# Kernel optimization log

Hardware: AMD Instinct MI355X
Metric: run time of the kernel (lower is better)

The kernel has to match this reference:

```python
import jax, jax.numpy as jnp
import numpy as np

B, D_IN, D_H, W_RANK, U_RANK = 8192, 1024, 2048, 256, 256


def setup_inputs() -> dict:
    key = jax.random.key(0)
    ks = jax.random.split(key, 6)
    return {
        "input": jax.random.normal(ks[0], (B, D_IN), dtype=jnp.float32),
        "state": jax.random.normal(ks[1], (B, D_H), dtype=jnp.float32),
        "W1": 0.1 * jax.random.normal(ks[2], (W_RANK, D_IN), dtype=jnp.float32),
        "W2": 0.1 * jax.random.normal(ks[3], (D_H, W_RANK), dtype=jnp.float32),
        "U1": 0.1 * jax.random.normal(ks[4], (U_RANK, D_H), dtype=jnp.float32),
        "U2": 0.1 * jax.random.normal(ks[5], (D_H, U_RANK), dtype=jnp.float32),
        "bias_gate": jnp.ones((1, D_H), dtype=jnp.float32),
        "bias_update": jnp.ones((1, D_H), dtype=jnp.float32),
        "zeta": 1.0 * jnp.ones((1, 1), dtype=jnp.float32),
        "nu": -4.0 * jnp.ones((1, 1), dtype=jnp.float32),
    }


def reference(input, state, W1, W2, U1, U2, bias_gate, bias_update, zeta, nu):
    # Low-rank projections: Wx = x @ W1^T @ W2^T ; Uh = h @ U1^T @ U2^T
    wx = jnp.einsum("bi,ri->br", input, W1)          # [B, wRank]
    wx = jnp.einsum("br,hr->bh", wx, W2)             # [B, H]
    uh = jnp.einsum("bh,rh->br", state, U1)          # [B, uRank]
    uh = jnp.einsum("br,hr->bh", uh, U2)             # [B, H]
    pre = wx + uh                                     # shared pre-activation
    z = jax.nn.sigmoid(pre + bias_gate)               # gate (sigmoid)
    h_cand = jnp.tanh(pre + bias_update)              # update (tanh)
    # h_t = z*h_{t-1} + (sigmoid(zeta)*(1-z) + sigmoid(nu)) * h_cand
    new_h = z * state + (jax.nn.sigmoid(zeta) * (1.0 - z) + jax.nn.sigmoid(nu)) * h_cand
    return new_h
```

## Files before the change

### kernel.cpp

```cpp
#include <hip/hip_runtime.h>
#include <hip/hip_fp16.h>
#include <cstdint>
#include <cstddef>


typedef _Float16 half8 __attribute__((ext_vector_type(8)));
typedef float f32x4 __attribute__((ext_vector_type(4)));

#define DIN 1024
#define DH 2048
#define RK 256
#define RB_LD 768
#define OFF_W1H 0
#define OFF_U1H 262144
#define OFF_W2H 786432
#define OFF_U2H 1310720

__device__ __forceinline__ half8 cvt8(const float4 a, const float4 b) {
  half8 h;
  h[0] = (_Float16)a.x; h[1] = (_Float16)a.y; h[2] = (_Float16)a.z; h[3] = (_Float16)a.w;
  h[4] = (_Float16)b.x; h[5] = (_Float16)b.y; h[6] = (_Float16)b.z; h[7] = (_Float16)b.w;
  return h;
}

__global__ __launch_bounds__(256)
void fgrnn_prep(const float* __restrict__ W1, const float* __restrict__ U1,
                const float* __restrict__ W2, const float* __restrict__ U2,
                _Float16* __restrict__ wb) {
  const int q = blockIdx.x * 256 + threadIdx.x;
  const float* src;
  int rel;
  if (q < 65536) { src = W1; rel = q; }
  else if (q < 196608) { src = U1; rel = q - 65536; }
  else if (q < 327680) { src = W2; rel = q - 196608; }
  else { src = U2; rel = q - 327680; }
  const float4 v = reinterpret_cast<const float4*>(src)[rel];
  union { _Float16 h[4]; uint2 u; } cv;
  cv.h[0] = (_Float16)v.x; cv.h[1] = (_Float16)v.y;
  cv.h[2] = (_Float16)v.z; cv.h[3] = (_Float16)v.w;
  reinterpret_cast<uint2*>(wb)[q] = cv.u;
}

__global__ __launch_bounds__(512)
void fgrnn_stage1(const float* __restrict__ x, const float* __restrict__ h,
                  const _Float16* __restrict__ wb, _Float16* __restrict__ rbuf) {
  const int bid = blockIdx.x;
  const int grp = bid >> 7;
  const int mtile = bid & 127;
  const float* A = grp ? h : x;
  const _Float16* Bw = grp ? (wb + OFF_U1H) : (wb + OFF_W1H);
  const int KA = grp ? DH : DIN;
  const int kbase = (grp == 2) ? 1024 : 0;
  const int colbase = grp << 8;
  const int row0 = mtile * 64;

  __shared__ _Float16 As[64 * 64];
  __shared__ _Float16 Bs[256 * 64];

  const int tid = threadIdx.x;
  const int lane = tid & 63;
  const int w = tid >> 6;
  const int wr = w >> 2, wc = w & 3;

  f32x4 acc[2][4];
#pragma unroll
  for (int i = 0; i < 2; ++i)
#pragma unroll
    for (int j = 0; j < 4; ++j) acc[i][j] = (f32x4){0.f, 0.f, 0.f, 0.f};

  const int sr = tid >> 3;
  const int sc = (tid & 7) * 8;

  float4 pa0, pa1;
  half8 pb[4];

  auto LOADG = [&](int it) {
    const int k0 = kbase + it * 64;
    const float* sa = A + (size_t)(row0 + sr) * KA + k0 + sc;
    pa0 = *reinterpret_cast<const float4*>(sa);
    pa1 = *reinterpret_cast<const float4*>(sa + 4);
#pragma unroll
    for (int j = 0; j < 4; ++j)
      pb[j] = *reinterpret_cast<const half8*>(Bw + (size_t)(j * 64 + sr) * KA + k0 + sc);
  };
  auto STORE = [&]() {
    *reinterpret_cast<half8*>(&As[sr * 64 + (sc ^ ((sr & 7) << 3))]) = cvt8(pa0, pa1);
#pragma unroll
    for (int j = 0; j < 4; ++j) {
      const int r = j * 64 + sr;
      *reinterpret_cast<half8*>(&Bs[r * 64 + (sc ^ ((r & 7) << 3))]) = pb[j];
    }
  };

  LOADG(0);
  STORE();
  __syncthreads();

  for (int it = 0; it < 16; ++it) {
    const bool more = (it + 1 < 16);
    if (more) LOADG(it + 1);
#pragma unroll
    for (int kk = 0; kk < 64; kk += 32) {
      half8 af[2], bf[4];
#pragma unroll
      for (int mi = 0; mi < 2; ++mi) {
        const int r = wr * 32 + mi * 16 + (lane & 15);
        af[mi] = *reinterpret_cast<const half8*>(
            &As[r * 64 + ((kk + 8 * (lane >> 4)) ^ ((r & 7) << 3))]);
      }
#pragma unroll
      for (int ni = 0; ni < 4; ++ni) {
        const int r = wc * 64 + ni * 16 + (lane & 15);
        bf[ni] = *reinterpret_cast<const half8*>(
            &Bs[r * 64 + ((kk + 8 * (lane >> 4)) ^ ((r & 7) << 3))]);
      }
#pragma unroll
      for (int mi = 0; mi < 2; ++mi)
#pragma unroll
        for (int ni = 0; ni < 4; ++ni)
          acc[mi][ni] =
              __builtin_amdgcn_mfma_f32_16x16x32_f16(af[mi], bf[ni], acc[mi][ni], 0, 0, 0);
    }
    if (more) {
      __syncthreads();
      STORE();
    }
    __syncthreads();
  }

#pragma unroll
  for (int mi = 0; mi < 2; ++mi)
#pragma unroll
    for (int ni = 0; ni < 4; ++ni)
#pragma unroll
      for (int e = 0; e < 4; ++e) {
        const int row = row0 + wr * 32 + mi * 16 + 4 * (lane >> 4) + e;
        const int col = colbase + wc * 64 + ni * 16 + (lane & 15);
        rbuf[(size_t)row * RB_LD + col] = (_Float16)acc[mi][ni][e];
      }
}

__global__ __launch_bounds__(256)
void fgrnn_stage2(const _Float16* __restrict__ rbuf, const _Float16* __restrict__ wb,
                  const float* __restrict__ state,
                  const float* __restrict__ bg, const float* __restrict__ bu,
                  const float* __restrict__ zeta, const float* __restrict__ nu,
                  float* __restrict__ out) {
  const int bid = blockIdx.x;
  const int mtile = bid >> 4;
  const int ntile = bid & 15;
  const int row0 = mtile * 64;
  const int col0 = ntile * 128;
  const _Float16* W2h = wb + OFF_W2H;
  const _Float16* U2h = wb + OFF_U2H;

  __shared__ _Float16 As[64 * 64];
  __shared__ _Float16 Bs[128 * 64];

  const int tid = threadIdx.x;
  const int lane = tid & 63;
  const int w = tid >> 6;
  const int wr = w >> 1, wc = w & 1;

  f32x4 acc[2][4];
#pragma unroll
  for (int i = 0; i < 2; ++i)
#pragma unroll
    for (int j = 0; j < 4; ++j) acc[i][j] = (f32x4){0.f, 0.f, 0.f, 0.f};

  const int sr = tid >> 3;
  const int sc = (tid & 7) * 8;

  half8 pa[2], pa2[2], pb[4];

  auto LOADG = [&](int it) {
    const int k0 = it * 64;
#pragma unroll
    for (int j = 0; j < 2; ++j) {
      const _Float16* p = rbuf + (size_t)(row0 + j * 32 + sr) * RB_LD + k0 + sc;
      pa[j] = *reinterpret_cast<const half8*>(p);
      if (k0 >= 256) pa2[j] = *reinterpret_cast<const half8*>(p + 256);
    }
    const _Float16* Bh = (k0 < 256) ? W2h : U2h;
    const int kb = k0 & 255;
#pragma unroll
    for (int j = 0; j < 4; ++j)
      pb[j] = *reinterpret_cast<const half8*>(Bh + (size_t)(col0 + j * 32 + sr) * RK + kb + sc);
  };
  auto STORE = [&](int it) {
    const int k0 = it * 64;
#pragma unroll
    for (int j = 0; j < 2; ++j) {
      const int r = j * 32 + sr;
      half8 v = pa[j];
      if (k0 >= 256) v = v + pa2[j];
      *reinterpret_cast<half8*>(&As[r * 64 + (sc ^ ((r & 7) << 3))]) = v;
    }
#pragma unroll
    for (int j = 0; j < 4; ++j) {
      const int r = j * 32 + sr;
      *reinterpret_cast<half8*>(&Bs[r * 64 + (sc ^ ((r & 7) << 3))]) = pb[j];
    }
  };

  LOADG(0);
  STORE(0);
  __syncthreads();

  for (int it = 0; it < 8; ++it) {
    const bool more = (it + 1 < 8);
    if (more) LOADG(it + 1);
#pragma unroll
    for (int kk = 0; kk < 64; kk += 32) {
      half8 af[2], bf[4];
#pragma unroll
      for (int mi = 0; mi < 2; ++mi) {
        const int r = wr * 32 + mi * 16 + (lane & 15);
        af[mi] = *reinterpret_cast<const half8*>(
            &As[r * 64 + ((kk + 8 * (lane >> 4)) ^ ((r & 7) << 3))]);
      }
#pragma unroll
      for (int ni = 0; ni < 4; ++ni) {
        const int r = wc * 64 + ni * 16 + (lane & 15);
        bf[ni] = *reinterpret_cast<const half8*>(
            &Bs[r * 64 + ((kk + 8 * (lane >> 4)) ^ ((r & 7) << 3))]);
      }
#pragma unroll
      for (int mi = 0; mi < 2; ++mi)
#pragma unroll
        for (int ni = 0; ni < 4; ++ni)
          acc[mi][ni] =
              __builtin_amdgcn_mfma_f32_16x16x32_f16(af[mi], bf[ni], acc[mi][ni], 0, 0, 0);
    }
    if (more) {
      __syncthreads();
      STORE(it + 1);
    }
    __syncthreads();
  }

  const float LOG2E = 1.44269504f;
  const float sz = __builtin_amdgcn_rcpf(1.f + __builtin_amdgcn_exp2f(-zeta[0] * LOG2E));
  const float sn = __builtin_amdgcn_rcpf(1.f + __builtin_amdgcn_exp2f(-nu[0] * LOG2E));
#pragma unroll
  for (int mi = 0; mi < 2; ++mi)
#pragma unroll
    for (int ni = 0; ni < 4; ++ni) {
      const int col = col0 + wc * 64 + ni * 16 + (lane & 15);
      const float bgc = bg[col];
      const float buc = bu[col];
#pragma unroll
      for (int e = 0; e < 4; ++e) {
        const int row = row0 + wr * 32 + mi * 16 + 4 * (lane >> 4) + e;
        const float pre = acc[mi][ni][e];
        const float zg =
            __builtin_amdgcn_rcpf(1.f + __builtin_amdgcn_exp2f(-(pre + bgc) * LOG2E));
        const float hc =
            1.f - 2.f * __builtin_amdgcn_rcpf(
                            1.f + __builtin_amdgcn_exp2f((pre + buc) * (2.f * LOG2E)));
        const float sv = state[(size_t)row * DH + col];
        out[(size_t)row * DH + col] = zg * sv + (sz * (1.f - zg) + sn) * hc;
      }
    }
}

extern "C" void kernel_launch(void* const* d_in, const int* in_sizes, int n_in,
                              void* d_out, int out_size, void* d_ws, size_t ws_size,
                              hipStream_t stream) {
  const float* input = (const float*)d_in[0];
  const float* state = (const float*)d_in[1];
  const float* W1 = (const float*)d_in[2];
  const float* W2 = (const float*)d_in[3];
  const float* U1 = (const float*)d_in[4];
  const float* U2 = (const float*)d_in[5];
  const float* bg = (const float*)d_in[6];
  const float* bu = (const float*)d_in[7];
  const float* zeta = (const float*)d_in[8];
  const float* nu = (const float*)d_in[9];
  float* out = (float*)d_out;
  _Float16* rbuf = (_Float16*)d_ws;
  _Float16* wb = (_Float16*)d_ws + (size_t)8192 * 768;

  fgrnn_prep<<<1792, 256, 0, stream>>>(W1, U1, W2, U2, wb);
  fgrnn_stage1<<<384, 512, 0, stream>>>(input, state, wb, rbuf);
  fgrnn_stage2<<<2048, 256, 0, stream>>>(rbuf, wb, state, bg, bu, zeta, nu, out);
}
```

Baseline: 77.87 us.

## Split stage1 K dimension into more partial groups with larger M tiles and XCD-aware block remap

```diff
diff --git a/kernel.cpp b/kernel.cpp
--- a/kernel.cpp
+++ b/kernel.cpp
@@ -10,11 +10,11 @@
 #define DIN 1024
 #define DH 2048
 #define RK 256
-#define RB_LD 768
 #define OFF_W1H 0
 #define OFF_U1H 262144
 #define OFF_W2H 786432
 #define OFF_U2H 1310720
+#define WB_HALVES 1835008
 
 __device__ __forceinline__ half8 cvt8(const float4 a, const float4 b) {
   half8 h;
@@ -41,20 +41,29 @@
   reinterpret_cast<uint2*>(wb)[q] = cv.u;
 }
 
+template <int G>
 __global__ __launch_bounds__(512)
 void fgrnn_stage1(const float* __restrict__ x, const float* __restrict__ h,
                   const _Float16* __restrict__ wb, _Float16* __restrict__ rbuf) {
+  constexpr int KL = (G == 6) ? 512 : 256;
+  constexpr int ITERS = KL / 64;
+  constexpr int GX = 1024 / KL;
+  constexpr int RBLD = G * 256;
+  constexpr int NB = G * 64;
+
   const int bid = blockIdx.x;
-  const int grp = bid >> 7;
-  const int mtile = bid & 127;
-  const float* A = grp ? h : x;
-  const _Float16* Bw = grp ? (wb + OFF_U1H) : (wb + OFF_W1H);
-  const int KA = grp ? DH : DIN;
-  const int kbase = (grp == 2) ? 1024 : 0;
-  const int colbase = grp << 8;
-  const int row0 = mtile * 64;
-
-  __shared__ _Float16 As[64 * 64];
+  const int L = (bid & 7) * (NB / 8) + (bid >> 3);
+  const int g = L >> 6;
+  const int mtile = L & 63;
+  const bool isx = g < GX;
+  const float* A = isx ? x : h;
+  const int KA = isx ? DIN : DH;
+  const int kbase = (isx ? g : (g - GX)) * KL;
+  const _Float16* Bw = wb + (isx ? OFF_W1H : OFF_U1H);
+  const int row0 = mtile * 128;
+  const int colbase = g * 256;
+
+  __shared__ _Float16 As[128 * 64];
   __shared__ _Float16 Bs[256 * 64];
 
   const int tid = threadIdx.x;
@@ -62,29 +71,37 @@
   const int w = tid >> 6;
   const int wr = w >> 2, wc = w & 3;
 
-  f32x4 acc[2][4];
-#pragma unroll
-  for (int i = 0; i < 2; ++i)
+  f32x4 acc[4][4];
+#pragma unroll
+  for (int i = 0; i < 4; ++i)
 #pragma unroll
     for (int j = 0; j < 4; ++j) acc[i][j] = (f32x4){0.f, 0.f, 0.f, 0.f};
 
   const int sr = tid >> 3;
   const int sc = (tid & 7) * 8;
 
-  float4 pa0, pa1;
+  float4 pa4[2][2];
   half8 pb[4];
 
   auto LOADG = [&](int it) {
     const int k0 = kbase + it * 64;
-    const float* sa = A + (size_t)(row0 + sr) * KA + k0 + sc;
-    pa0 = *reinterpret_cast<const float4*>(sa);
-    pa1 = *reinterpret_cast<const float4*>(sa + 4);
+#pragma unroll
+    for (int j = 0; j < 2; ++j) {
+      const float* s = A + (size_t)(row0 + j * 64 + sr) * KA + k0 + sc;
+      pa4[j][0] = *reinterpret_cast<const float4*>(s);
+      pa4[j][1] = *reinterpret_cast<const float4*>(s + 4);
+    }
 #pragma unroll
     for (int j = 0; j < 4; ++j)
       pb[j] = *reinterpret_cast<const half8*>(Bw + (size_t)(j * 64 + sr) * KA + k0 + sc);
   };
   auto STORE = [&]() {
-    *reinterpret_cast<half8*>(&As[sr * 64 + (sc ^ ((sr & 7) << 3))]) = cvt8(pa0, pa1);
+#pragma unroll
+    for (int j = 0; j < 2; ++j) {
+      const int r = j * 64 + sr;
+      *reinterpret_cast<half8*>(&As[r * 64 + (sc ^ ((r & 7) << 3))]) =
+          cvt8(pa4[j][0], pa4[j][1]);
+    }
 #pragma unroll
     for (int j = 0; j < 4; ++j) {
       const int r = j * 64 + sr;
@@ -96,15 +113,15 @@
   STORE();
   __syncthreads();
 
-  for (int it = 0; it < 16; ++it) {
-    const bool more = (it + 1 < 16);
+  for (int it = 0; it < ITERS; ++it) {
+    const bool more = (it + 1 < ITERS);
     if (more) LOADG(it + 1);
 #pragma unroll
     for (int kk = 0; kk < 64; kk += 32) {
-      half8 af[2], bf[4];
-#pragma unroll
-      for (int mi = 0; mi < 2; ++mi) {
-        const int r = wr * 32 + mi * 16 + (lane & 15);
+      half8 af[4], bf[4];
+#pragma unroll
+      for (int mi = 0; mi < 4; ++mi) {
+        const int r = wr * 64 + mi * 16 + (lane & 15);
         af[mi] = *reinterpret_cast<const half8*>(
             &As[r * 64 + ((kk + 8 * (lane >> 4)) ^ ((r & 7) << 3))]);
       }
@@ -115,7 +132,7 @@
             &Bs[r * 64 + ((kk + 8 * (lane >> 4)) ^ ((r & 7) << 3))]);
       }
 #pragma unroll
-      for (int mi = 0; mi < 2; ++mi)
+      for (int mi = 0; mi < 4; ++mi)
 #pragma unroll
         for (int ni = 0; ni < 4; ++ni)
           acc[mi][ni] =
@@ -129,26 +146,32 @@
   }
 
 #pragma unroll
-  for (int mi = 0; mi < 2; ++mi)
+  for (int mi = 0; mi < 4; ++mi)
 #pragma unroll
     for (int ni = 0; ni < 4; ++ni)
 #pragma unroll
       for (int e = 0; e < 4; ++e) {
-        const int row = row0 + wr * 32 + mi * 16 + 4 * (lane >> 4) + e;
+        const int row = row0 + wr * 64 + mi * 16 + 4 * (lane >> 4) + e;
         const int col = colbase + wc * 64 + ni * 16 + (lane & 15);
-        rbuf[(size_t)row * RB_LD + col] = (_Float16)acc[mi][ni][e];
-      }
-}
-
+        rbuf[(size_t)row * RBLD + col] = (_Float16)acc[mi][ni][e];
+      }
+}
+
+template <int G>
 __global__ __launch_bounds__(256)
 void fgrnn_stage2(const _Float16* __restrict__ rbuf, const _Float16* __restrict__ wb,
                   const float* __restrict__ state,
                   const float* __restrict__ bg, const float* __restrict__ bu,
                   const float* __restrict__ zeta, const float* __restrict__ nu,
                   float* __restrict__ out) {
+  constexpr int GX = (G == 6) ? 2 : 4;
+  constexpr int GH = G - GX;
+  constexpr int RBLD = G * 256;
+
   const int bid = blockIdx.x;
-  const int mtile = bid >> 4;
-  const int ntile = bid & 15;
+  const int L = (bid & 7) * 256 + (bid >> 3);
+  const int mtile = L >> 4;
+  const int ntile = L & 15;
   const int row0 = mtile * 64;
   const int col0 = ntile * 128;
   const _Float16* W2h = wb + OFF_W2H;
@@ -171,17 +194,22 @@
   const int sr = tid >> 3;
   const int sc = (tid & 7) * 8;
 
-  half8 pa[2], pa2[2], pb[4];
+  half8 pa[2][GH];
+  half8 pb[4];
 
   auto LOADG = [&](int it) {
     const int k0 = it * 64;
+    const bool iswx = (k0 < 256);
+    const int cb = iswx ? k0 : (GX * 256 + (k0 - 256));
+    const int np = iswx ? GX : GH;
 #pragma unroll
     for (int j = 0; j < 2; ++j) {
-      const _Float16* p = rbuf + (size_t)(row0 + j * 32 + sr) * RB_LD + k0 + sc;
-      pa[j] = *reinterpret_cast<const half8*>(p);
-      if (k0 >= 256) pa2[j] = *reinterpret_cast<const half8*>(p + 256);
-    }
-    const _Float16* Bh = (k0 < 256) ? W2h : U2h;
+      const _Float16* p = rbuf + (size_t)(row0 + j * 32 + sr) * RBLD + cb + sc;
+#pragma unroll
+      for (int q = 0; q < GH; ++q)
+        if (q < np) pa[j][q] = *reinterpret_cast<const half8*>(p + q * 256);
+    }
+    const _Float16* Bh = iswx ? W2h : U2h;
     const int kb = k0 & 255;
 #pragma unroll
     for (int j = 0; j < 4; ++j)
@@ -189,11 +217,14 @@
   };
   auto STORE = [&](int it) {
     const int k0 = it * 64;
+    const int np = (k0 < 256) ? GX : GH;
 #pragma unroll
     for (int j = 0; j < 2; ++j) {
+      half8 v = pa[j][0];
+#pragma unroll
+      for (int q = 1; q < GH; ++q)
+        if (q < np) v = v + pa[j][q];
       const int r = j * 32 + sr;
-      half8 v = pa[j];
-      if (k0 >= 256) v = v + pa2[j];
       *reinterpret_cast<half8*>(&As[r * 64 + (sc ^ ((r & 7) << 3))]) = v;
     }
 #pragma unroll
@@ -278,10 +309,19 @@
   const float* zeta = (const float*)d_in[8];
   const float* nu = (const float*)d_in[9];
   float* out = (float*)d_out;
+
+  const size_t need12 = ((size_t)8192 * 3072 + WB_HALVES) * 2;
   _Float16* rbuf = (_Float16*)d_ws;
-  _Float16* wb = (_Float16*)d_ws + (size_t)8192 * 768;
-
-  fgrnn_prep<<<1792, 256, 0, stream>>>(W1, U1, W2, U2, wb);
-  fgrnn_stage1<<<384, 512, 0, stream>>>(input, state, wb, rbuf);
-  fgrnn_stage2<<<2048, 256, 0, stream>>>(rbuf, wb, state, bg, bu, zeta, nu, out);
-}
+
+  if (ws_size >= need12) {
+    _Float16* wb = rbuf + (size_t)8192 * 3072;
+    fgrnn_prep<<<1792, 256, 0, stream>>>(W1, U1, W2, U2, wb);
+    fgrnn_stage1<12><<<768, 512, 0, stream>>>(input, state, wb, rbuf);
+    fgrnn_stage2<12><<<2048, 256, 0, stream>>>(rbuf, wb, state, bg, bu, zeta, nu, out);
+  } else {
+    _Float16* wb = rbuf + (size_t)8192 * 1536;
+    fgrnn_prep<<<1792, 256, 0, stream>>>(W1, U1, W2, U2, wb);
+    fgrnn_stage1<6><<<384, 512, 0, stream>>>(input, state, wb, rbuf);
+    fgrnn_stage2<6><<<2048, 256, 0, stream>>>(rbuf, wb, state, bg, bu, zeta, nu, out);
+  }
+}
```

Result: slower. 101.7 us (+30.6%).

## Double-buffer stage1 LDS, enlarge state-GEMM M tiles, swizzle stage2 block order

Applied to the files above, without the earlier changes.

```diff
diff --git a/kernel.cpp b/kernel.cpp
--- a/kernel.cpp
+++ b/kernel.cpp
@@ -10,11 +10,12 @@
 #define DIN 1024
 #define DH 2048
 #define RK 256
-#define RB_LD 768
+#define RBLD 768
 #define OFF_W1H 0
 #define OFF_U1H 262144
 #define OFF_W2H 786432
 #define OFF_U2H 1310720
+#define WB_HALVES 1835008
 
 __device__ __forceinline__ half8 cvt8(const float4 a, const float4 b) {
   half8 h;
@@ -41,103 +42,135 @@
   reinterpret_cast<uint2*>(wb)[q] = cv.u;
 }
 
-__global__ __launch_bounds__(512)
-void fgrnn_stage1(const float* __restrict__ x, const float* __restrict__ h,
-                  const _Float16* __restrict__ wb, _Float16* __restrict__ rbuf) {
-  const int bid = blockIdx.x;
-  const int grp = bid >> 7;
-  const int mtile = bid & 127;
-  const float* A = grp ? h : x;
-  const _Float16* Bw = grp ? (wb + OFF_U1H) : (wb + OFF_W1H);
-  const int KA = grp ? DH : DIN;
-  const int kbase = (grp == 2) ? 1024 : 0;
-  const int colbase = grp << 8;
-  const int row0 = mtile * 64;
-
-  __shared__ _Float16 As[64 * 64];
-  __shared__ _Float16 Bs[256 * 64];
+template <int MI>
+__device__ __forceinline__ void s1_body(
+    const float* __restrict__ A, const int KA, const int kbase,
+    const _Float16* __restrict__ Bw, _Float16* __restrict__ rbuf,
+    const int row0, const int colbase,
+    _Float16* __restrict__ AsBase, _Float16* __restrict__ BsBase) {
+  constexpr int APASS = MI / 2;
+  constexpr int ASTRIDE = MI * 32 * 64;
+  constexpr int BSTRIDE = 256 * 64;
 
   const int tid = threadIdx.x;
   const int lane = tid & 63;
   const int w = tid >> 6;
   const int wr = w >> 2, wc = w & 3;
-
-  f32x4 acc[2][4];
-#pragma unroll
-  for (int i = 0; i < 2; ++i)
-#pragma unroll
-    for (int j = 0; j < 4; ++j) acc[i][j] = (f32x4){0.f, 0.f, 0.f, 0.f};
-
   const int sr = tid >> 3;
   const int sc = (tid & 7) * 8;
 
-  float4 pa0, pa1;
-  half8 pb[4];
-
-  auto LOADG = [&](int it) {
+  f32x4 acc[MI][4];
+#pragma unroll
+  for (int i = 0; i < MI; ++i)
+#pragma unroll
+    for (int j = 0; j < 4; ++j) acc[i][j] = (f32x4){0.f, 0.f, 0.f, 0.f};
+
+  float4 raE[APASS][2], raO[APASS][2];
+  half8 rbE[4], rbO[4];
+
+  auto LOADG = [&](float4 (&ra)[APASS][2], half8 (&rb)[4], int it) {
     const int k0 = kbase + it * 64;
-    const float* sa = A + (size_t)(row0 + sr) * KA + k0 + sc;
-    pa0 = *reinterpret_cast<const float4*>(sa);
-    pa1 = *reinterpret_cast<const float4*>(sa + 4);
+#pragma unroll
+    for (int j = 0; j < APASS; ++j) {
+      const float* s = A + (size_t)(row0 + j * 64 + sr) * KA + k0 + sc;
+      ra[j][0] = *reinterpret_cast<const float4*>(s);
+      ra[j][1] = *reinterpret_cast<const float4*>(s + 4);
+    }
 #pragma unroll
     for (int j = 0; j < 4; ++j)
-      pb[j] = *reinterpret_cast<const half8*>(Bw + (size_t)(j * 64 + sr) * KA + k0 + sc);
-  };
-  auto STORE = [&]() {
-    *reinterpret_cast<half8*>(&As[sr * 64 + (sc ^ ((sr & 7) << 3))]) = cvt8(pa0, pa1);
+      rb[j] = *reinterpret_cast<const half8*>(Bw + (size_t)(j * 64 + sr) * KA + k0 + sc);
+  };
+  auto STORE = [&](const float4 (&ra)[APASS][2], const half8 (&rb)[4],
+                   _Float16* as, _Float16* bs) {
+#pragma unroll
+    for (int j = 0; j < APASS; ++j) {
+      const int r = j * 64 + sr;
+      *reinterpret_cast<half8*>(&as[r * 64 + (sc ^ ((r & 7) << 3))]) =
+          cvt8(ra[j][0], ra[j][1]);
+    }
 #pragma unroll
     for (int j = 0; j < 4; ++j) {
       const int r = j * 64 + sr;
-      *reinterpret_cast<half8*>(&Bs[r * 64 + (sc ^ ((r & 7) << 3))]) = pb[j];
-    }
-  };
-
-  LOADG(0);
-  STORE();
-  __syncthreads();
-
-  for (int it = 0; it < 16; ++it) {
-    const bool more = (it + 1 < 16);
-    if (more) LOADG(it + 1);
+      *reinterpret_cast<half8*>(&bs[r * 64 + (sc ^ ((r & 7) << 3))]) = rb[j];
+    }
+  };
+  auto COMPUTE = [&](const _Float16* as, const _Float16* bs) {
 #pragma unroll
     for (int kk = 0; kk < 64; kk += 32) {
-      half8 af[2], bf[4];
-#pragma unroll
-      for (int mi = 0; mi < 2; ++mi) {
-        const int r = wr * 32 + mi * 16 + (lane & 15);
+      half8 af[MI], bf[4];
+#pragma unroll
+      for (int mi = 0; mi < MI; ++mi) {
+        const int r = wr * (MI * 16) + mi * 16 + (lane & 15);
         af[mi] = *reinterpret_cast<const half8*>(
-            &As[r * 64 + ((kk + 8 * (lane >> 4)) ^ ((r & 7) << 3))]);
+            &as[r * 64 + ((kk + 8 * (lane >> 4)) ^ ((r & 7) << 3))]);
       }
 #pragma unroll
       for (int ni = 0; ni < 4; ++ni) {
         const int r = wc * 64 + ni * 16 + (lane & 15);
         bf[ni] = *reinterpret_cast<const half8*>(
-            &Bs[r * 64 + ((kk + 8 * (lane >> 4)) ^ ((r & 7) << 3))]);
-      }
-#pragma unroll
-      for (int mi = 0; mi < 2; ++mi)
+            &bs[r * 64 + ((kk + 8 * (lane >> 4)) ^ ((r & 7) << 3))]);
+      }
+#pragma unroll
+      for (int mi = 0; mi < MI; ++mi)
 #pragma unroll
         for (int ni = 0; ni < 4; ++ni)
           acc[mi][ni] =
               __builtin_amdgcn_mfma_f32_16x16x32_f16(af[mi], bf[ni], acc[mi][ni], 0, 0, 0);
     }
-    if (more) {
-      __syncthreads();
-      STORE();
-    }
-    __syncthreads();
+  };
+  auto BAR = [&]() {
+    asm volatile("s_waitcnt lgkmcnt(0)" ::: "memory");
+    __builtin_amdgcn_s_barrier();
+    asm volatile("" ::: "memory");
+  };
+
+  _Float16* as0 = AsBase;
+  _Float16* as1 = AsBase + ASTRIDE;
+  _Float16* bs0 = BsBase;
+  _Float16* bs1 = BsBase + BSTRIDE;
+
+  LOADG(raE, rbE, 0);
+  LOADG(raO, rbO, 1);
+  STORE(raE, rbE, as0, bs0);
+  BAR();
+
+#pragma unroll 1
+  for (int it2 = 0; it2 < 16; it2 += 2) {
+    if (it2 + 2 < 16) LOADG(raE, rbE, it2 + 2);
+    COMPUTE(as0, bs0);
+    STORE(raO, rbO, as1, bs1);
+    BAR();
+    if (it2 + 3 < 16) LOADG(raO, rbO, it2 + 3);
+    COMPUTE(as1, bs1);
+    if (it2 + 2 < 16) STORE(raE, rbE, as0, bs0);
+    BAR();
   }
 
 #pragma unroll
-  for (int mi = 0; mi < 2; ++mi)
+  for (int mi = 0; mi < MI; ++mi)
 #pragma unroll
     for (int ni = 0; ni < 4; ++ni)
 #pragma unroll
       for (int e = 0; e < 4; ++e) {
-        const int row = row0 + wr * 32 + mi * 16 + 4 * (lane >> 4) + e;
+        const int row = row0 + wr * (MI * 16) + mi * 16 + 4 * (lane >> 4) + e;
         const int col = colbase + wc * 64 + ni * 16 + (lane & 15);
-        rbuf[(size_t)row * RB_LD + col] = (_Float16)acc[mi][ni][e];
-      }
+        rbuf[(size_t)row * RBLD + col] = (_Float16)acc[mi][ni][e];
+      }
+}
+
+__global__ __launch_bounds__(512)
+void fgrnn_stage1(const float* __restrict__ x, const float* __restrict__ h,
+                  const _Float16* __restrict__ wb, _Float16* __restrict__ rbuf) {
+  __shared__ _Float16 As[2 * 128 * 64];
+  __shared__ _Float16 Bs[2 * 256 * 64];
+  const int bid = blockIdx.x;
+  if (bid < 128) {
+    s1_body<2>(x, DIN, 0, wb + OFF_W1H, rbuf, bid * 64, 0, As, Bs);
+  } else if (bid < 192) {
+    s1_body<4>(h, DH, 0, wb + OFF_U1H, rbuf, (bid - 128) * 128, 256, As, Bs);
+  } else {
+    s1_body<4>(h, DH, 1024, wb + OFF_U1H, rbuf, (bid - 192) * 128, 512, As, Bs);
+  }
 }
 
 __global__ __launch_bounds__(256)
@@ -147,8 +180,9 @@
                   const float* __restrict__ zeta, const float* __restrict__ nu,
                   float* __restrict__ out) {
   const int bid = blockIdx.x;
-  const int mtile = bid >> 4;
-  const int ntile = bid & 15;
+  const int L = (bid & 7) * 256 + (bid >> 3);
+  const int mtile = L >> 4;
+  const int ntile = L & 15;
   const int row0 = mtile * 64;
   const int col0 = ntile * 128;
   const _Float16* W2h = wb + OFF_W2H;
@@ -175,13 +209,14 @@
 
   auto LOADG = [&](int it) {
     const int k0 = it * 64;
+    const bool iswx = (k0 < 256);
 #pragma unroll
     for (int j = 0; j < 2; ++j) {
-      const _Float16* p = rbuf + (size_t)(row0 + j * 32 + sr) * RB_LD + k0 + sc;
+      const _Float16* p = rbuf + (size_t)(row0 + j * 32 + sr) * RBLD + k0 + sc;
       pa[j] = *reinterpret_cast<const half8*>(p);
-      if (k0 >= 256) pa2[j] = *reinterpret_cast<const half8*>(p + 256);
-    }
-    const _Float16* Bh = (k0 < 256) ? W2h : U2h;
+      if (!iswx) pa2[j] = *reinterpret_cast<const half8*>(p + 256);
+    }
+    const _Float16* Bh = iswx ? W2h : U2h;
     const int kb = k0 & 255;
 #pragma unroll
     for (int j = 0; j < 4; ++j)
@@ -191,9 +226,9 @@
     const int k0 = it * 64;
 #pragma unroll
     for (int j = 0; j < 2; ++j) {
-      const int r = j * 32 + sr;
       half8 v = pa[j];
       if (k0 >= 256) v = v + pa2[j];
+      const int r = j * 32 + sr;
       *reinterpret_cast<half8*>(&As[r * 64 + (sc ^ ((r & 7) << 3))]) = v;
     }
 #pragma unroll
@@ -278,10 +313,11 @@
   const float* zeta = (const float*)d_in[8];
   const float* nu = (const float*)d_in[9];
   float* out = (float*)d_out;
+
   _Float16* rbuf = (_Float16*)d_ws;
-  _Float16* wb = (_Float16*)d_ws + (size_t)8192 * 768;
+  _Float16* wb = rbuf + (size_t)8192 * RBLD;
 
   fgrnn_prep<<<1792, 256, 0, stream>>>(W1, U1, W2, U2, wb);
-  fgrnn_stage1<<<384, 512, 0, stream>>>(input, state, wb, rbuf);
+  fgrnn_stage1<<<256, 512, 0, stream>>>(input, state, wb, rbuf);
   fgrnn_stage2<<<2048, 256, 0, stream>>>(rbuf, wb, state, bg, bu, zeta, nu, out);
 }
```

Result: faster. 69.03 us (-11.4%).

## Retile stage1 with K=128 steps, pre-tiled weights and XCD-aware block mapping

Applied to the files above, without the earlier changes.

```diff
diff --git a/kernel.cpp b/kernel.cpp
--- a/kernel.cpp
+++ b/kernel.cpp
@@ -10,9 +10,9 @@
 #define DIN 1024
 #define DH 2048
 #define RK 256
-#define RB_LD 768
-#define OFF_W1H 0
-#define OFF_U1H 262144
+#define RBLD 768
+#define OFF_W1T 0
+#define OFF_U1T 262144
 #define OFF_W2H 786432
 #define OFF_U2H 1310720
 
@@ -28,116 +28,221 @@
                 const float* __restrict__ W2, const float* __restrict__ U2,
                 _Float16* __restrict__ wb) {
   const int q = blockIdx.x * 256 + threadIdx.x;
-  const float* src;
-  int rel;
-  if (q < 65536) { src = W1; rel = q; }
-  else if (q < 196608) { src = U1; rel = q - 65536; }
-  else if (q < 327680) { src = W2; rel = q - 196608; }
-  else { src = U2; rel = q - 327680; }
-  const float4 v = reinterpret_cast<const float4*>(src)[rel];
-  union { _Float16 h[4]; uint2 u; } cv;
-  cv.h[0] = (_Float16)v.x; cv.h[1] = (_Float16)v.y;
-  cv.h[2] = (_Float16)v.z; cv.h[3] = (_Float16)v.w;
-  reinterpret_cast<uint2*>(wb)[q] = cv.u;
-}
-
-__global__ __launch_bounds__(512)
+  float4 v;
+  int o;
+  if (q < 65536) {
+    v = reinterpret_cast<const float4*>(W1)[q];
+    const int e = q * 4, r = e >> 10, k = e & 1023;
+    o = OFF_W1T + (k >> 7) * 32768 + r * 128 + (k & 127);
+  } else if (q < 196608) {
+    const int qq = q - 65536;
+    v = reinterpret_cast<const float4*>(U1)[qq];
+    const int e = qq * 4, r = e >> 11, k = e & 2047;
+    o = OFF_U1T + (k >> 7) * 32768 + r * 128 + (k & 127);
+  } else if (q < 327680) {
+    const int qq = q - 196608;
+    v = reinterpret_cast<const float4*>(W2)[qq];
+    o = OFF_W2H + qq * 4;
+  } else {
+    const int qq = q - 327680;
+    v = reinterpret_cast<const float4*>(U2)[qq];
+    o = OFF_U2H + qq * 4;
+  }
+  union { _Float16 hh[4]; uint2 u; } cv;
+  cv.hh[0] = (_Float16)v.x; cv.hh[1] = (_Float16)v.y;
+  cv.hh[2] = (_Float16)v.z; cv.hh[3] = (_Float16)v.w;
+  *reinterpret_cast<uint2*>(wb + o) = cv.u;
+}
+
+__global__ __launch_bounds__(512, 4)
 void fgrnn_stage1(const float* __restrict__ x, const float* __restrict__ h,
                   const _Float16* __restrict__ wb, _Float16* __restrict__ rbuf) {
+  __shared__ _Float16 As[64 * 128];
+  __shared__ _Float16 Bs[256 * 128];
+
   const int bid = blockIdx.x;
-  const int grp = bid >> 7;
-  const int mtile = bid & 127;
-  const float* A = grp ? h : x;
-  const _Float16* Bw = grp ? (wb + OFF_U1H) : (wb + OFF_W1H);
-  const int KA = grp ? DH : DIN;
-  const int kbase = (grp == 2) ? 1024 : 0;
-  const int colbase = grp << 8;
-  const int row0 = mtile * 64;
-
-  __shared__ _Float16 As[64 * 64];
-  __shared__ _Float16 Bs[256 * 64];
-
+  const int L = (bid & 7) * 64 + (bid >> 3);
   const int tid = threadIdx.x;
   const int lane = tid & 63;
-  const int w = tid >> 6;
-  const int wr = w >> 2, wc = w & 3;
-
-  f32x4 acc[2][4];
-#pragma unroll
-  for (int i = 0; i < 2; ++i)
-#pragma unroll
-    for (int j = 0; j < 4; ++j) acc[i][j] = (f32x4){0.f, 0.f, 0.f, 0.f};
-
-  const int sr = tid >> 3;
-  const int sc = (tid & 7) * 8;
-
-  float4 pa0, pa1;
-  half8 pb[4];
-
-  auto LOADG = [&](int it) {
-    const int k0 = kbase + it * 64;
-    const float* sa = A + (size_t)(row0 + sr) * KA + k0 + sc;
-    pa0 = *reinterpret_cast<const float4*>(sa);
-    pa1 = *reinterpret_cast<const float4*>(sa + 4);
-#pragma unroll
-    for (int j = 0; j < 4; ++j)
-      pb[j] = *reinterpret_cast<const half8*>(Bw + (size_t)(j * 64 + sr) * KA + k0 + sc);
-  };
-  auto STORE = [&]() {
-    *reinterpret_cast<half8*>(&As[sr * 64 + (sc ^ ((sr & 7) << 3))]) = cvt8(pa0, pa1);
-#pragma unroll
-    for (int j = 0; j < 4; ++j) {
-      const int r = j * 64 + sr;
-      *reinterpret_cast<half8*>(&Bs[r * 64 + (sc ^ ((r & 7) << 3))]) = pb[j];
-    }
-  };
-
-  LOADG(0);
-  STORE();
-  __syncthreads();
-
-  for (int it = 0; it < 16; ++it) {
-    const bool more = (it + 1 < 16);
-    if (more) LOADG(it + 1);
-#pragma unroll
-    for (int kk = 0; kk < 64; kk += 32) {
-      half8 af[2], bf[4];
-#pragma unroll
-      for (int mi = 0; mi < 2; ++mi) {
-        const int r = wr * 32 + mi * 16 + (lane & 15);
-        af[mi] = *reinterpret_cast<const half8*>(
-            &As[r * 64 + ((kk + 8 * (lane >> 4)) ^ ((r & 7) << 3))]);
-      }
-#pragma unroll
-      for (int ni = 0; ni < 4; ++ni) {
-        const int r = wc * 64 + ni * 16 + (lane & 15);
-        bf[ni] = *reinterpret_cast<const half8*>(
-            &Bs[r * 64 + ((kk + 8 * (lane >> 4)) ^ ((r & 7) << 3))]);
-      }
-#pragma unroll
-      for (int mi = 0; mi < 2; ++mi)
-#pragma unroll
-        for (int ni = 0; ni < 4; ++ni)
-          acc[mi][ni] =
-              __builtin_amdgcn_mfma_f32_16x16x32_f16(af[mi], bf[ni], acc[mi][ni], 0, 0, 0);
-    }
-    if (more) {
+  const int wv = tid >> 6;
+
+  if (L < 256) {
+    const int row0 = L * 32;
+    const _Float16* Wt = wb + OFF_W1T;
+
+    f32x4 acc[2][2];
+#pragma unroll
+    for (int i = 0; i < 2; ++i)
+#pragma unroll
+      for (int j = 0; j < 2; ++j) acc[i][j] = (f32x4){0.f, 0.f, 0.f, 0.f};
+
+    const int sr = tid >> 4;
+    const int sg = (tid & 15) * 8;
+
+    float4 pa0, pa1;
+    half8 pbx[8];
+
+    auto LOADG = [&](int it) {
+      const float* s = x + (size_t)(row0 + sr) * DIN + it * 128 + sg;
+      pa0 = *reinterpret_cast<const float4*>(s);
+      pa1 = *reinterpret_cast<const float4*>(s + 4);
+      const _Float16* bsrc = Wt + it * 32768 + tid * 8;
+#pragma unroll
+      for (int i = 0; i < 8; ++i)
+        pbx[i] = *reinterpret_cast<const half8*>(bsrc + i * 4096);
+    };
+    auto STORE = [&]() {
+      *reinterpret_cast<half8*>(&As[sr * 128 + (sg ^ ((sr & 7) << 3))]) = cvt8(pa0, pa1);
+#pragma unroll
+      for (int i = 0; i < 8; ++i) {
+        const int idx = tid + i * 512;
+        const int r = idx >> 4, c = (idx & 15) * 8;
+        *reinterpret_cast<half8*>(&Bs[r * 128 + (c ^ ((r & 7) << 3))]) = pbx[i];
+      }
+    };
+
+    LOADG(0);
+    STORE();
+    __syncthreads();
+
+    for (int it = 0; it < 8; ++it) {
+      const bool more = (it + 1 < 8);
+      if (more) LOADG(it + 1);
+#pragma unroll
+      for (int kk = 0; kk < 128; kk += 32) {
+        half8 af[2], bf[2];
+#pragma unroll
+        for (int mi = 0; mi < 2; ++mi) {
+          const int r = mi * 16 + (lane & 15);
+          af[mi] = *reinterpret_cast<const half8*>(
+              &As[r * 128 + ((kk + 8 * (lane >> 4)) ^ ((r & 7) << 3))]);
+        }
+#pragma unroll
+        for (int ni = 0; ni < 2; ++ni) {
+          const int r = wv * 32 + ni * 16 + (lane & 15);
+          bf[ni] = *reinterpret_cast<const half8*>(
+              &Bs[r * 128 + ((kk + 8 * (lane >> 4)) ^ ((r & 7) << 3))]);
+        }
+#pragma unroll
+        for (int mi = 0; mi < 2; ++mi)
+#pragma unroll
+          for (int ni = 0; ni < 2; ++ni)
+            acc[mi][ni] =
+                __builtin_amdgcn_mfma_f32_16x16x32_f16(af[mi], bf[ni], acc[mi][ni], 0, 0, 0);
+      }
+      if (more) {
+        __syncthreads();
+        STORE();
+      }
       __syncthreads();
-      STORE();
-    }
+    }
+
+#pragma unroll
+    for (int mi = 0; mi < 2; ++mi)
+#pragma unroll
+      for (int ni = 0; ni < 2; ++ni)
+#pragma unroll
+        for (int e = 0; e < 4; ++e) {
+          const int row = row0 + mi * 16 + 4 * (lane >> 4) + e;
+          const int col = wv * 32 + ni * 16 + (lane & 15);
+          rbuf[(size_t)row * RBLD + col] = (_Float16)acc[mi][ni][e];
+        }
+  } else {
+    const int r6 = L - 256;
+    const int kp = r6 >> 7;
+    const int mtile = r6 & 127;
+    const int row0 = mtile * 64;
+    const _Float16* Ut = wb + OFF_U1T + kp * 8 * 32768;
+    const int kofs = kp * 1024;
+    const int colbase = 256 + kp * 256;
+    const int wr = wv >> 2, wc = wv & 3;
+
+    f32x4 acc[2][4];
+#pragma unroll
+    for (int i = 0; i < 2; ++i)
+#pragma unroll
+      for (int j = 0; j < 4; ++j) acc[i][j] = (f32x4){0.f, 0.f, 0.f, 0.f};
+
+    float4 pa0[2], pa1[2];
+    half8 pbx[8];
+
+    auto LOADG = [&](int it) {
+#pragma unroll
+      for (int j = 0; j < 2; ++j) {
+        const int idx = tid + j * 512;
+        const int r = idx >> 4, g = (idx & 15) * 8;
+        const float* s = h + (size_t)(row0 + r) * DH + kofs + it * 128 + g;
+        pa0[j] = *reinterpret_cast<const float4*>(s);
+        pa1[j] = *reinterpret_cast<const float4*>(s + 4);
+      }
+      const _Float16* bsrc = Ut + it * 32768 + tid * 8;
+#pragma unroll
+      for (int i = 0; i < 8; ++i)
+        pbx[i] = *reinterpret_cast<const half8*>(bsrc + i * 4096);
+    };
+    auto STORE = [&]() {
+#pragma unroll
+      for (int j = 0; j < 2; ++j) {
+        const int idx = tid + j * 512;
+        const int r = idx >> 4, c = (idx & 15) * 8;
+        *reinterpret_cast<half8*>(&As[r * 128 + (c ^ ((r & 7) << 3))]) =
+            cvt8(pa0[j], pa1[j]);
+      }
+#pragma unroll
+      for (int i = 0; i < 8; ++i) {
+        const int idx = tid + i * 512;
+        const int r = idx >> 4, c = (idx & 15) * 8;
+        *reinterpret_cast<half8*>(&Bs[r * 128 + (c ^ ((r & 7) << 3))]) = pbx[i];
+      }
+    };
+
+    LOADG(0);
+    STORE();
     __syncthreads();
+
+    for (int it = 0; it < 8; ++it) {
+      const bool more = (it + 1 < 8);
+      if (more) LOADG(it + 1);
+#pragma unroll
+      for (int kk = 0; kk < 128; kk += 32) {
+        half8 af[2], bf[4];
+#pragma unroll
+        for (int mi = 0; mi < 2; ++mi) {
+          const int r = wr * 32 + mi * 16 + (lane & 15);
+          af[mi] = *reinterpret_cast<const half8*>(
+              &As[r * 128 + ((kk + 8 * (lane >> 4)) ^ ((r & 7) << 3))]);
+        }
+#pragma unroll
+        for (int ni = 0; ni < 4; ++ni) {
+          const int r = wc * 64 + ni * 16 + (lane & 15);
+          bf[ni] = *reinterpret_cast<const half8*>(
+              &Bs[r * 128 + ((kk + 8 * (lane >> 4)) ^ ((r & 7) << 3))]);
+        }
+#pragma unroll
+        for (int mi = 0; mi < 2; ++mi)
+#pragma unroll
+          for (int ni = 0; ni < 4; ++ni)
+            acc[mi][ni] =
+                __builtin_amdgcn_mfma_f32_16x16x32_f16(af[mi], bf[ni], acc[mi][ni], 0, 0, 0);
+      }
+      if (more) {
+        __syncthreads();
+        STORE();
+      }
+      __syncthreads();
+    }
+
+#pragma unroll
+    for (int mi = 0; mi < 2; ++mi)
+#pragma unroll
+      for (int ni = 0; ni < 4; ++ni)
+#pragma unroll
+        for (int e = 0; e < 4; ++e) {
+          const int row = row0 + wr * 32 + mi * 16 + 4 * (lane >> 4) + e;
+          const int col = colbase + wc * 64 + ni * 16 + (lane & 15);
+          rbuf[(size_t)row * RBLD + col] = (_Float16)acc[mi][ni][e];
+        }
   }
-
-#pragma unroll
-  for (int mi = 0; mi < 2; ++mi)
-#pragma unroll
-    for (int ni = 0; ni < 4; ++ni)
-#pragma unroll
-      for (int e = 0; e < 4; ++e) {
-        const int row = row0 + wr * 32 + mi * 16 + 4 * (lane >> 4) + e;
-        const int col = colbase + wc * 64 + ni * 16 + (lane & 15);
-        rbuf[(size_t)row * RB_LD + col] = (_Float16)acc[mi][ni][e];
-      }
 }
 
 __global__ __launch_bounds__(256)
@@ -147,8 +252,9 @@
                   const float* __restrict__ zeta, const float* __restrict__ nu,
                   float* __restrict__ out) {
   const int bid = blockIdx.x;
-  const int mtile = bid >> 4;
-  const int ntile = bid & 15;
+  const int L = (bid & 7) * 256 + (bid >> 3);
+  const int mtile = L >> 4;
+  const int ntile = L & 15;
   const int row0 = mtile * 64;
   const int col0 = ntile * 128;
   const _Float16* W2h = wb + OFF_W2H;
@@ -175,13 +281,14 @@
 
   auto LOADG = [&](int it) {
     const int k0 = it * 64;
+    const bool iswx = (k0 < 256);
 #pragma unroll
     for (int j = 0; j < 2; ++j) {
-      const _Float16* p = rbuf + (size_t)(row0 + j * 32 + sr) * RB_LD + k0 + sc;
+      const _Float16* p = rbuf + (size_t)(row0 + j * 32 + sr) * RBLD + k0 + sc;
       pa[j] = *reinterpret_cast<const half8*>(p);
-      if (k0 >= 256) pa2[j] = *reinterpret_cast<const half8*>(p + 256);
-    }
-    const _Float16* Bh = (k0 < 256) ? W2h : U2h;
+      if (!iswx) pa2[j] = *reinterpret_cast<const half8*>(p + 256);
+    }
+    const _Float16* Bh = iswx ? W2h : U2h;
     const int kb = k0 & 255;
 #pragma unroll
     for (int j = 0; j < 4; ++j)
@@ -191,9 +298,9 @@
     const int k0 = it * 64;
 #pragma unroll
     for (int j = 0; j < 2; ++j) {
-      const int r = j * 32 + sr;
       half8 v = pa[j];
       if (k0 >= 256) v = v + pa2[j];
+      const int r = j * 32 + sr;
       *reinterpret_cast<half8*>(&As[r * 64 + (sc ^ ((r & 7) << 3))]) = v;
     }
 #pragma unroll
@@ -278,10 +385,11 @@
   const float* zeta = (const float*)d_in[8];
   const float* nu = (const float*)d_in[9];
   float* out = (float*)d_out;
+
   _Float16* rbuf = (_Float16*)d_ws;
-  _Float16* wb = (_Float16*)d_ws + (size_t)8192 * 768;
+  _Float16* wb = rbuf + (size_t)8192 * RBLD;
 
   fgrnn_prep<<<1792, 256, 0, stream>>>(W1, U1, W2, U2, wb);
-  fgrnn_stage1<<<384, 512, 0, stream>>>(input, state, wb, rbuf);
+  fgrnn_stage1<<<512, 512, 0, stream>>>(input, state, wb, rbuf);
   fgrnn_stage2<<<2048, 256, 0, stream>>>(rbuf, wb, state, bg, bu, zeta, nu, out);
 }
```

Measured after the change: 78.54 us. About the same (+0.9%).
